# Kernel tuning notes

Hardware: AMD Instinct MI355X
Metric: run time of the kernel (lower is better)

Reference implementation:

```python
import jax, jax.numpy as jnp
import numpy as np

BS = 128          # block_size for weight scales
FP8_MAX = 448.0   # e4m3fn max


def setup_inputs() -> dict:
    key = jax.random.key(0)
    k1, k2, k3 = jax.random.split(key, 3)
    T, I, O = 8192, 4096, 6144  # tokens, input_size, output_size
    x = jax.random.normal(k1, (T, I), dtype=jnp.float32)
    # weight is stored as fp8 in the module; we generate fp32 and cast inside reference
    weight = jax.random.normal(k2, (O, I), dtype=jnp.float32) * 0.02
    weight_scale_inv = jax.random.uniform(k3, (O // BS, I // BS), dtype=jnp.float32,
                                          minval=0.5, maxval=1.5)
    return {"x": x, "weight": weight, "weight_scale_inv": weight_scale_inv}


def reference(x, weight, weight_scale_inv):
    # --- stored fp8 weight (module keeps weight in float8_e4m3fn) ---
    w_fp8 = weight.astype(jnp.float8_e4m3fn)
    O, I = w_fp8.shape
    # --- block-wise dequantization: W_deq[o,i] = w[o,i] * scale[o//BS, i//BS] ---
    w_deq = (w_fp8.astype(jnp.float32)
             .reshape(O // BS, BS, I // BS, BS)
             * weight_scale_inv[:, None, :, None]).reshape(O, I)
    # --- dynamic per-token fp8 quantization of activations ---
    amax = jnp.clip(jnp.max(jnp.abs(x), axis=-1, keepdims=True), 1e-12, None)
    x_scale = (amax / FP8_MAX).astype(jnp.float32)   # [T, 1]
    x_fp8 = (x / x_scale).astype(jnp.float8_e4m3fn)  # [T, I]
    # --- GEMM on dequantized operands: out = (x_fp8 * x_scale) @ W_deq^T ---
    out = (x_fp8.astype(jnp.float32) @ w_deq.T) * x_scale  # [T, O]
    return out
```

## Files before the change

### kernel.cpp

```cpp
#include <hip/hip_runtime.h>
#include <stdint.h>

#define T_TOK 8192
#define K_IN  4096
#define O_OUT 6144

typedef __attribute__((ext_vector_type(4))) float f32x4;
typedef __attribute__((ext_vector_type(8))) int i32x8;
typedef unsigned int uint32;


__device__ inline void load_lds_16(const void* g, void* l) {
    __builtin_amdgcn_global_load_lds(
        (const __attribute__((address_space(1))) unsigned int*)g,
        (__attribute__((address_space(3))) unsigned int*)l, 16, 0, 0);
}

__device__ inline int pack4_fp8(float a, float b, float c, float d) {
    int r = __builtin_amdgcn_cvt_pk_fp8_f32(a, b, 0, false);
    r = __builtin_amdgcn_cvt_pk_fp8_f32(c, d, r, true);
    return r;
}

__global__ __launch_bounds__(256) void quant_x(const float* __restrict__ x,
                                               uint32* __restrict__ xq,
                                               float* __restrict__ xscale) {
    const int t   = blockIdx.x;
    const int tid = threadIdx.x;
    const float4* row4 = (const float4*)(x + (size_t)t * K_IN);

    float4 v[4];
    float amax = 0.f;
#pragma unroll
    for (int j = 0; j < 4; ++j) {
        v[j] = row4[tid + j * 256];
        amax = fmaxf(amax, fmaxf(fmaxf(fabsf(v[j].x), fabsf(v[j].y)),
                                 fmaxf(fabsf(v[j].z), fabsf(v[j].w))));
    }
#pragma unroll
    for (int off = 32; off > 0; off >>= 1)
        amax = fmaxf(amax, __shfl_down(amax, off, 64));
    __shared__ float red[4];
    if ((tid & 63) == 0) red[tid >> 6] = amax;
    __syncthreads();
    amax = fmaxf(fmaxf(red[0], red[1]), fmaxf(red[2], red[3]));

    const float scale = fmaxf(amax, 1e-12f) / 448.0f;
    if (tid == 0) xscale[t] = scale;

    uint32* orow = xq + (size_t)t * (K_IN / 4);
#pragma unroll
    for (int j = 0; j < 4; ++j) {
        float q0 = v[j].x / scale, q1 = v[j].y / scale;
        float q2 = v[j].z / scale, q3 = v[j].w / scale;
        orow[tid + j * 256] = (uint32)pack4_fp8(q0, q1, q2, q3);
    }
}

__global__ __launch_bounds__(256) void quant_w(const float* __restrict__ w,
                                               uint32* __restrict__ wq) {
    const size_t u = (size_t)blockIdx.x * 256 + threadIdx.x;
    float4 v = ((const float4*)w)[u];
    wq[u] = (uint32)pack4_fp8(v.x, v.y, v.z, v.w);
}

__global__ __launch_bounds__(512, 2) void gemm_fp8(const unsigned char* __restrict__ A,
                                                   const unsigned char* __restrict__ B,
                                                   const float* __restrict__ sinv,
                                                   const float* __restrict__ xscale,
                                                   float* __restrict__ C) {
    constexpr int BM = 256, BN = 256, BK = 128;
    constexpr int NKB = K_IN / BK;
    extern __shared__ unsigned char smem[];

    const int bn  = blockIdx.x;
    const int bm  = blockIdx.y;
    const int tid = threadIdx.x;
    const int lane = tid & 63;
    const int wv   = tid >> 6;
    const int wm   = (wv >> 2) * 128;
    const int wn   = (wv & 3) * 64;
    const int G2   = (lane >> 4) * 2;

    const int tr = tid >> 3;
    const int kc = (tid & 7) ^ (tr & 7);
    const unsigned char* Ag = A + (size_t)(bm * BM + tr) * K_IN + kc * 16;
    const int ldst = tid * 16;

    const int rA  = lane & 15;
    const int cs0 = ((G2    ) ^ (lane & 7)) * 16;
    const int cs1 = ((G2 + 1) ^ (lane & 7)) * 16;

    const unsigned char* Bg = B + (size_t)(bn * BN + wn + rA) * K_IN + G2 * 16;

    const float* srow = sinv + (size_t)(bn * 2 + (wn >> 7)) * NKB;

    union F { i32x8 v; int4 h[2]; };
    f32x4 acc[8][4] = {};
    F bA[4], bB[4];
    float s_prev = srow[0];

#define STAGE(ck_) {                                                         \
    unsigned char* d_ = smem + (size_t)((ck_) & 3) * 32768 + ldst;           \
    const unsigned char* g_ = Ag + (size_t)((ck_) & 31) * BK;                \
    load_lds_16(g_,                      d_);                                \
    load_lds_16(g_ + (size_t) 64 * K_IN, d_ +  8192);                        \
    load_lds_16(g_ + (size_t)128 * K_IN, d_ + 16384);                        \
    load_lds_16(g_ + (size_t)192 * K_IN, d_ + 24576); }

#define LOADB(dst_, ck_) {                                                   \
    const unsigned char* g_ = Bg + (size_t)((ck_) & 31) * BK;                \
    dst_[0].h[0] = *(const int4*)(g_);                                       \
    dst_[0].h[1] = *(const int4*)(g_ + 16);                                  \
    dst_[1].h[0] = *(const int4*)(g_ + (size_t)16 * K_IN);                   \
    dst_[1].h[1] = *(const int4*)(g_ + (size_t)16 * K_IN + 16);              \
    dst_[2].h[0] = *(const int4*)(g_ + (size_t)32 * K_IN);                   \
    dst_[2].h[1] = *(const int4*)(g_ + (size_t)32 * K_IN + 16);              \
    dst_[3].h[0] = *(const int4*)(g_ + (size_t)48 * K_IN);                   \
    dst_[3].h[1] = *(const int4*)(g_ + (size_t)48 * K_IN + 16); }

#define LDA(d_, i_, pA_) {                                                   \
    const unsigned char* q_ = (pA_) + (wm + (i_) * 16 + rA) * 128;           \
    (d_).h[0] = *(const int4*)(q_ + cs0);                                    \
    (d_).h[1] = *(const int4*)(q_ + cs1); }

#define MFMA(i_, j_, af_, bf_)                                               \
    acc[i_][j_] = __builtin_amdgcn_mfma_scale_f32_16x16x128_f8f6f4(          \
        (af_).v, (bf_).v, acc[i_][j_], 0 , 0 ,             \
        0, 0x7f7f7f7f, 0, 0x7f7f7f7f);

#define KB_BODY(kb_, bcur_, bnxt_) {                                         \
    const unsigned char* pA = smem + (size_t)((kb_) & 3) * 32768;            \
    const float s_cur = srow[kb_];                                           \
    const float rr = s_prev / s_cur;               \
    s_prev = s_cur;                                                          \
    LOADB(bnxt_, (kb_) + 1);                                                 \
    STAGE((kb_) + 3);                                                        \
    __builtin_amdgcn_s_setprio(1);                                           \
    _Pragma("unroll")                                                        \
    for (int i = 0; i < 8; ++i) {                                            \
        F af; LDA(af, i, pA);                                                \
        acc[i][0] *= rr; acc[i][1] *= rr; acc[i][2] *= rr; acc[i][3] *= rr;  \
        MFMA(i, 0, af, bcur_[0]); MFMA(i, 1, af, bcur_[1]);                  \
        MFMA(i, 2, af, bcur_[2]); MFMA(i, 3, af, bcur_[3]);                  \
    }                                                                        \
    __builtin_amdgcn_s_setprio(0);                                           \
    __syncthreads(); }

    LOADB(bA, 0);
    STAGE(0); STAGE(1); STAGE(2);
    __syncthreads();

    for (int kb = 0; kb < NKB; kb += 2) {
        KB_BODY(kb,     bA, bB);
        KB_BODY(kb + 1, bB, bA);
    }

#pragma unroll
    for (int i = 0; i < 8; ++i) {
#pragma unroll
        for (int r = 0; r < 4; ++r) {
            const int m_g = bm * BM + wm + i * 16 + (lane >> 4) * 4 + r;
            const float f = xscale[m_g] * s_prev;
            float* crow = C + (size_t)m_g * O_OUT + bn * BN + wn;
#pragma unroll
            for (int j = 0; j < 4; ++j)
                crow[j * 16 + (lane & 15)] = acc[i][j][r] * f;
        }
    }
#undef STAGE
#undef LOADB
#undef LDA
#undef MFMA
#undef KB_BODY
}

extern "C" void kernel_launch(void* const* d_in, const int* in_sizes, int n_in,
                              void* d_out, int out_size, void* d_ws, size_t ws_size,
                              hipStream_t stream) {
    const float* x    = (const float*)d_in[0];
    const float* w    = (const float*)d_in[1];
    const float* sinv = (const float*)d_in[2];
    float* out = (float*)d_out;

    char* ws = (char*)d_ws;
    uint32* xq = (uint32*)ws;
    uint32* wq = (uint32*)(ws + (size_t)T_TOK * K_IN);
    float* xscale = (float*)(ws + (size_t)T_TOK * K_IN
                                + (size_t)O_OUT * K_IN);

    quant_x<<<T_TOK, 256, 0, stream>>>(x, xq, xscale);
    quant_w<<<(O_OUT * K_IN) / (4 * 256), 256, 0, stream>>>(w, wq);
    dim3 grid(O_OUT / 256, T_TOK / 256);
    gemm_fp8<<<grid, 512, 131072 , stream>>>(
        (const unsigned char*)xq, (const unsigned char*)wq, sinv, xscale, out);
}
```

Before: 648.8 us.

## Shrink GEMM tile to 128x128 with 4 waves and double-buffered LDS

Shrinks the FP8 GEMM block tile from 256x256 to 128x128, uses 256 threads (4 waves) per block and cuts LDS from a 4-stage 128KB ring to a 2-stage 32KB double buffer. B-fragment prefetch is dropped: B is now loaded in the same iteration it is consumed, and the loop is no longer unrolled by two. The aim is more blocks per CU and a simpler schedule. In exchange it halves the reuse of each loaded tile, roughly doubling global traffic, and exposes more latency through the shallower pipeline and the missing B prefetch.

```diff
diff --git a/kernel.cpp b/kernel.cpp
--- a/kernel.cpp
+++ b/kernel.cpp
@@ -64,12 +64,12 @@
     wq[u] = (uint32)pack4_fp8(v.x, v.y, v.z, v.w);
 }
 
-__global__ __launch_bounds__(512, 2) void gemm_fp8(const unsigned char* __restrict__ A,
+__global__ __launch_bounds__(256, 3) void gemm_fp8(const unsigned char* __restrict__ A,
                                                    const unsigned char* __restrict__ B,
                                                    const float* __restrict__ sinv,
                                                    const float* __restrict__ xscale,
                                                    float* __restrict__ C) {
-    constexpr int BM = 256, BN = 256, BK = 128;
+    constexpr int BM = 128, BN = 128, BK = 128;
     constexpr int NKB = K_IN / BK;
     extern __shared__ unsigned char smem[];
 
@@ -78,8 +78,8 @@
     const int tid = threadIdx.x;
     const int lane = tid & 63;
     const int wv   = tid >> 6;
-    const int wm   = (wv >> 2) * 128;
-    const int wn   = (wv & 3) * 64;
+    const int wm   = (wv >> 1) * 64;
+    const int wn   = (wv & 1) * 64;
     const int G2   = (lane >> 4) * 2;
 
     const int tr = tid >> 3;
@@ -93,23 +93,22 @@
 
     const unsigned char* Bg = B + (size_t)(bn * BN + wn + rA) * K_IN + G2 * 16;
 
-    const float* srow = sinv + (size_t)(bn * 2 + (wn >> 7)) * NKB;
+    const float* srow = sinv + (size_t)bn * NKB;
 
     union F { i32x8 v; int4 h[2]; };
-    f32x4 acc[8][4] = {};
-    F bA[4], bB[4];
+    f32x4 acc[4][4] = {};
     float s_prev = srow[0];
 
 #define STAGE(ck_) {                                                         \
-    unsigned char* d_ = smem + (size_t)((ck_) & 3) * 32768 + ldst;           \
+    unsigned char* d_ = smem + (size_t)((ck_) & 1) * 16384 + ldst;           \
     const unsigned char* g_ = Ag + (size_t)((ck_) & 31) * BK;                \
     load_lds_16(g_,                      d_);                                \
+    load_lds_16(g_ + (size_t) 32 * K_IN, d_ +  4096);                        \
     load_lds_16(g_ + (size_t) 64 * K_IN, d_ +  8192);                        \
-    load_lds_16(g_ + (size_t)128 * K_IN, d_ + 16384);                        \
-    load_lds_16(g_ + (size_t)192 * K_IN, d_ + 24576); }
+    load_lds_16(g_ + (size_t) 96 * K_IN, d_ + 12288); }
 
 #define LOADB(dst_, ck_) {                                                   \
-    const unsigned char* g_ = Bg + (size_t)((ck_) & 31) * BK;                \
+    const unsigned char* g_ = Bg + (size_t)(ck_) * BK;                       \
     dst_[0].h[0] = *(const int4*)(g_);                                       \
     dst_[0].h[1] = *(const int4*)(g_ + 16);                                  \
     dst_[1].h[0] = *(const int4*)(g_ + (size_t)16 * K_IN);                   \
@@ -129,35 +128,38 @@
         (af_).v, (bf_).v, acc[i_][j_], 0 , 0 ,             \
         0, 0x7f7f7f7f, 0, 0x7f7f7f7f);
 
-#define KB_BODY(kb_, bcur_, bnxt_) {                                         \
-    const unsigned char* pA = smem + (size_t)((kb_) & 3) * 32768;            \
-    const float s_cur = srow[kb_];                                           \
-    const float rr = s_prev / s_cur;               \
-    s_prev = s_cur;                                                          \
-    LOADB(bnxt_, (kb_) + 1);                                                 \
-    STAGE((kb_) + 3);                                                        \
-    __builtin_amdgcn_s_setprio(1);                                           \
-    _Pragma("unroll")                                                        \
-    for (int i = 0; i < 8; ++i) {                                            \
-        F af; LDA(af, i, pA);                                                \
-        acc[i][0] *= rr; acc[i][1] *= rr; acc[i][2] *= rr; acc[i][3] *= rr;  \
-        MFMA(i, 0, af, bcur_[0]); MFMA(i, 1, af, bcur_[1]);                  \
-        MFMA(i, 2, af, bcur_[2]); MFMA(i, 3, af, bcur_[3]);                  \
-    }                                                                        \
-    __builtin_amdgcn_s_setprio(0);                                           \
-    __syncthreads(); }
-
-    LOADB(bA, 0);
-    STAGE(0); STAGE(1); STAGE(2);
+    STAGE(0);
     __syncthreads();
 
-    for (int kb = 0; kb < NKB; kb += 2) {
-        KB_BODY(kb,     bA, bB);
-        KB_BODY(kb + 1, bB, bA);
+    for (int kb = 0; kb < NKB; ++kb) {
+        const unsigned char* pA = smem + (size_t)(kb & 1) * 16384;
+        const float s_cur = srow[kb];
+        const float rr = s_prev / s_cur;
+        s_prev = s_cur;
+
+        F b[4];
+        LOADB(b, kb);
+        STAGE(kb + 1);
+
+#pragma unroll
+        for (int i = 0; i < 4; ++i) {
+            acc[i][0] *= rr; acc[i][1] *= rr;
+            acc[i][2] *= rr; acc[i][3] *= rr;
+        }
+
+        __builtin_amdgcn_s_setprio(1);
+#pragma unroll
+        for (int i = 0; i < 4; ++i) {
+            F af; LDA(af, i, pA);
+            MFMA(i, 0, af, b[0]); MFMA(i, 1, af, b[1]);
+            MFMA(i, 2, af, b[2]); MFMA(i, 3, af, b[3]);
+        }
+        __builtin_amdgcn_s_setprio(0);
+        __syncthreads();
     }
 
 #pragma unroll
-    for (int i = 0; i < 8; ++i) {
+    for (int i = 0; i < 4; ++i) {
 #pragma unroll
         for (int r = 0; r < 4; ++r) {
             const int m_g = bm * BM + wm + i * 16 + (lane >> 4) * 4 + r;
@@ -172,7 +174,6 @@
 #undef LOADB
 #undef LDA
 #undef MFMA
-#undef KB_BODY
 }
 
 extern "C" void kernel_launch(void* const* d_in, const int* in_sizes, int n_in,
@@ -191,7 +192,7 @@
 
     quant_x<<<T_TOK, 256, 0, stream>>>(x, xq, xscale);
     quant_w<<<(O_OUT * K_IN) / (4 * 256), 256, 0, stream>>>(w, wq);
-    dim3 grid(O_OUT / 256, T_TOK / 256);
-    gemm_fp8<<<grid, 512, 131072 , stream>>>(
+    dim3 grid(O_OUT / 128, T_TOK / 128);
+    gemm_fp8<<<grid, 256, 32768 , stream>>>(
         (const unsigned char*)xq, (const unsigned char*)wq, sinv, xscale, out);
 }
```

Result: slower. 731.8 us (+12.8%).
